# Performance work log

Measured on AMD Instinct MI355X. Metric: run time of the kernel, lower is better.

Reference implementation:

```python
import jax, jax.numpy as jnp
import numpy as np
import math

D_INPUT = 1024
D_Q = 1024
D_K = 1024
D_V = 1024
D_MODEL = 1024
B, S = 4, 2048


def setup_inputs() -> dict:
    key = jax.random.key(0)
    ks = jax.random.split(key, 9)
    sc = 0.02
    return {
        "x": jax.random.normal(ks[0], (B, S, D_INPUT), dtype=jnp.float32),
        "wq": jax.random.normal(ks[1], (D_INPUT, D_Q), dtype=jnp.float32) * sc,
        "bq": jnp.zeros((D_Q,), dtype=jnp.float32),
        "wk": jax.random.normal(ks[2], (D_INPUT, D_K), dtype=jnp.float32) * sc,
        "bk": jnp.zeros((D_K,), dtype=jnp.float32),
        "wv": jax.random.normal(ks[3], (D_INPUT, D_V), dtype=jnp.float32) * sc,
        "bv": jnp.zeros((D_V,), dtype=jnp.float32),
        "wp": jax.random.normal(ks[4], (D_V, D_MODEL), dtype=jnp.float32) * sc,
        "bp": jnp.zeros((D_MODEL,), dtype=jnp.float32),
    }


def reference(x, wq, bq, wk, bk, wv, bv, wp, bp):
    scale = math.sqrt(D_K)  # NOTE: original MULTIPLIES by sqrt(d_k)
    q = x @ wq + bq  # [B,S,Dq]
    k = x @ wk + bk  # [B,S,Dk]
    v = x @ wv + bv  # [B,S,Dv]
    scores = jnp.einsum('bsd,btd->bst', q, k) * scale
    p_attn = jax.nn.softmax(scores, axis=-1)
    # dropout: inference mode (training=False) -> identity
    context = jnp.einsum('bst,btd->bsd', p_attn, v)
    output = context @ wp + bp
    return (output, p_attn)
```

## Files before the change

kernel.cpp:

```cpp
#include <hip/hip_runtime.h>

typedef unsigned short u16;
typedef short bf16x8 __attribute__((ext_vector_type(8)));
typedef float floatx4 __attribute__((ext_vector_type(4)));

static __device__ __forceinline__ u16 f2bf(float f) {
  unsigned int u = __float_as_uint(f);
  unsigned int lsb = (u >> 16) & 1u;
  u += 0x7FFFu + lsb;
  return (u16)(u >> 16);
}
static __device__ __forceinline__ float bf2f(u16 u) {
  return __uint_as_float(((unsigned int)u) << 16);
}

static __device__ __forceinline__ void gl_lds16(const u16* g, u16* l) {
  __builtin_amdgcn_global_load_lds(
      (const __attribute__((address_space(1))) void*)g,
      (__attribute__((address_space(3))) void*)l, 16, 0, 0);
}

__global__ __launch_bounds__(256)
void prep_weights(const float* __restrict__ wq, const float* __restrict__ wk,
                  const float* __restrict__ wv, const float* __restrict__ wp,
                  const float* __restrict__ bq, const float* __restrict__ bk,
                  const float* __restrict__ bv,
                  u16* __restrict__ qkvThi, u16* __restrict__ qkvTlo,
                  u16* __restrict__ wpThi, float* __restrict__ bqkv) {
  __shared__ float t[32][33];
  const int z = blockIdx.z;
  const int tid = threadIdx.x;
  if (z == 4) {
    if (blockIdx.y == 0 && blockIdx.x < 12) {
      const int i = blockIdx.x * 256 + tid;
      bqkv[i] = (i < 1024) ? bq[i] : (i < 2048) ? bk[i - 1024] : bv[i - 2048];
    }
    return;
  }
  const float* in = (z == 0) ? wq : (z == 1) ? wk : (z == 2) ? wv : wp;
  u16* hi = (z == 3) ? wpThi : (qkvThi + (size_t)z * 1024 * 1024);
  u16* lo = (z == 0) ? qkvTlo : (z == 1) ? (qkvTlo + 1024 * 1024) : (u16*)nullptr;
  const int want_lo = (z < 2);

  const int r0 = blockIdx.y * 32, c0 = blockIdx.x * 32;
  const int lr = tid >> 3;
  const int lc = (tid & 7) * 4;
  float4 v = *(const float4*)(in + (size_t)(r0 + lr) * 1024 + c0 + lc);
  t[lr][lc + 0] = v.x; t[lr][lc + 1] = v.y; t[lr][lc + 2] = v.z; t[lr][lc + 3] = v.w;
  __syncthreads();
  u16 ph[4], pl[4];
#pragma unroll
  for (int j = 0; j < 4; j++) {
    float f = t[lc + j][lr];
    ph[j] = f2bf(f);
    pl[j] = f2bf(f - bf2f(ph[j]));
  }
  const size_t o = (size_t)(c0 + lr) * 1024 + r0 + lc;
  *(uint2*)(hi + o) = *(uint2*)ph;
  if (want_lo) *(uint2*)(lo + o) = *(uint2*)pl;
}

__global__ __launch_bounds__(256)
void split_f32(const float* __restrict__ in, u16* __restrict__ hi,
               u16* __restrict__ lo) {
  const size_t i4 = ((size_t)blockIdx.x * 256 + threadIdx.x) * 4;
  float4 v = *(const float4*)(in + i4);
  float f[4] = {v.x, v.y, v.z, v.w};
  u16 ph[4], pl[4];
#pragma unroll
  for (int j = 0; j < 4; j++) {
    ph[j] = f2bf(f[j]);
    pl[j] = f2bf(f[j] - bf2f(ph[j]));
  }
  *(uint2*)(hi + i4) = *(uint2*)ph;
  *(uint2*)(lo + i4) = *(uint2*)pl;
}

template<int KB, int ASP, int BSP, int OM, int HB>
__global__ __launch_bounds__(256)
void gemm_mfma(const u16* __restrict__ Ahi, const u16* __restrict__ Alo,
               const u16* __restrict__ Bhi, const u16* __restrict__ Blo,
               const float* __restrict__ bias,
               void* __restrict__ C0, void* __restrict__ C1,
               void* __restrict__ C2, void* __restrict__ C3,
               void* __restrict__ C4,
               int N, int K, int lda, int ldb, int ldc,
               long long aB, long long bB, long long cB, float scale,
               int nsplit) {
  constexpr int CM = KB / 8 - 1;
  constexpr int RPI = 512 / KB;
  constexpr int NI = KB / 16;
  constexpr int PL = 128 * KB;
  __shared__ __align__(16) u16 As[(1 + ASP) * PL];
  __shared__ __align__(16) u16 Bs[(1 + BSP) * PL];

  const int bz = blockIdx.z;
  const u16* A0 = Ahi + (size_t)bz * aB;
  const u16* A1 = ASP ? (Alo + (size_t)bz * aB) : (const u16*)nullptr;
  const u16* B0 = Bhi + (size_t)bz * bB;
  const u16* B1 = BSP ? (Blo + (size_t)bz * bB) : (const u16*)nullptr;

  const int m0 = blockIdx.y * 128;
  const int n0 = blockIdx.x * 128;
  const bool bsplit = (ASP && BSP) ? (n0 < nsplit) : false;
  const int tid = threadIdx.x;
  const int w = tid >> 6;
  const int L = tid & 63;
  const int rr = L & 15, quad = L >> 4;
  const int wm = (w >> 1) * 64, wn = (w & 1) * 64;

  const int lrow = (KB == 32) ? (L >> 2) : (L >> 3);
  const int c3 = (L & CM) ^ ((L >> 3) & CM);
  const int srow = w * 32 + lrow;
  u16* stA = &As[w * 32 * KB];
  u16* stB = &Bs[w * 32 * KB];
  const u16* gA0 = A0 + (size_t)(m0 + srow) * lda + c3 * 8;
  const u16* gA1 = ASP ? A1 + (size_t)(m0 + srow) * lda + c3 * 8 : (const u16*)nullptr;
  const u16* gB0 = B0 + (size_t)(n0 + srow) * ldb + c3 * 8;
  const u16* gB1 = BSP ? B1 + (size_t)(n0 + srow) * ldb + c3 * 8 : (const u16*)nullptr;

  floatx4 acc[4][4] = {};

  for (int k0 = 0; k0 < K; k0 += KB) {
#pragma unroll
    for (int q = 0; q < NI; q++) {
      gl_lds16(gA0 + k0 + (size_t)q * RPI * lda, stA + q * 512);
      gl_lds16(gB0 + k0 + (size_t)q * RPI * ldb, stB + q * 512);
    }
    if (ASP && bsplit) {
#pragma unroll
      for (int q = 0; q < NI; q++)
        gl_lds16(gA1 + k0 + (size_t)q * RPI * lda, stA + PL + q * 512);
    }
    if (BSP && bsplit) {
#pragma unroll
      for (int q = 0; q < NI; q++)
        gl_lds16(gB1 + k0 + (size_t)q * RPI * ldb, stB + PL + q * 512);
    }
    __syncthreads();

#pragma unroll
    for (int s = 0; s < KB / 32; s++) {
      const int pcb = (KB == 32) ? (quad ^ ((rr >> 1) & 3)) * 8
                                 : ((s * 4 + quad) ^ (rr & 7)) * 8;
      bf16x8 a0[4], a1[4], b0[4], b1[4];
#pragma unroll
      for (int i = 0; i < 4; i++) {
        const int arow = wm + i * 16 + rr;
        const int brow = wn + i * 16 + rr;
        a0[i] = *(const bf16x8*)&As[arow * KB + pcb];
        b0[i] = *(const bf16x8*)&Bs[brow * KB + pcb];
        if (ASP && BSP) {
          if (bsplit) {
            a1[i] = *(const bf16x8*)&As[PL + arow * KB + pcb];
            b1[i] = *(const bf16x8*)&Bs[PL + brow * KB + pcb];
          }
        }
      }
#pragma unroll
      for (int i = 0; i < 4; i++) {
#pragma unroll
        for (int j = 0; j < 4; j++) {
          acc[i][j] = __builtin_amdgcn_mfma_f32_16x16x32_bf16(a0[i], b0[j], acc[i][j], 0, 0, 0);
          if (ASP && BSP) {
            if (bsplit) {
              acc[i][j] = __builtin_amdgcn_mfma_f32_16x16x32_bf16(a0[i], b1[j], acc[i][j], 0, 0, 0);
              acc[i][j] = __builtin_amdgcn_mfma_f32_16x16x32_bf16(a1[i], b0[j], acc[i][j], 0, 0, 0);
            }
          }
        }
      }
    }
    __syncthreads();
  }

#pragma unroll
  for (int i = 0; i < 4; i++) {
    const int mbase = m0 + wm + i * 16 + quad * 4;
#pragma unroll
    for (int j = 0; j < 4; j++) {
      const int col = n0 + wn + j * 16 + rr;
      float bvs = 0.f;
      if (HB) bvs = bias[col];
      if (OM == 4) {
        if (col < 2048) {
          u16* hi; u16* lo;
          if (col < 1024) { hi = (u16*)C0; lo = (u16*)C1; }
          else            { hi = (u16*)C2; lo = (u16*)C3; }
          const int cc = col & 1023;
#pragma unroll
          for (int ii = 0; ii < 4; ii++) {
            const float v = acc[i][j][ii] + bvs;
            const size_t idx = (size_t)(mbase + ii) * 1024 + cc;
            const u16 h = f2bf(v);
            hi[idx] = h;
            lo[idx] = f2bf(v - bf2f(h));
          }
        } else {
          const int d = col - 2048;
          u16 pk[4];
#pragma unroll
          for (int ii = 0; ii < 4; ii++) pk[ii] = f2bf(acc[i][j][ii] + bvs);
          const size_t idx = (size_t)(mbase >> 11) * (2048 * 1024) +
                             (size_t)d * 2048 + (mbase & 2047);
          *(uint2*)((u16*)C4 + idx) = *(uint2*)pk;
        }
      } else {
        u16* Cb = (u16*)C0 + (size_t)bz * cB;
        float* Cf = (float*)C0 + (size_t)bz * cB;
#pragma unroll
        for (int ii = 0; ii < 4; ii++) {
          const float v = acc[i][j][ii] * scale + bvs;
          const size_t idx = (size_t)(mbase + ii) * ldc + col;
          if (OM == 0) Cb[idx] = f2bf(v);
          else         Cf[idx] = v;
        }
      }
    }
  }
}

__global__ __launch_bounds__(256)
void softmax_rows(float* __restrict__ S, u16* __restrict__ Pb) {
  const int row = blockIdx.x;
  float* s = S + (size_t)row * 2048;
  const int tid = threadIdx.x;
  const int w = tid >> 6;
  __shared__ float redm[4];
  __shared__ float reds[4];

  float v[8];
  float mx = -1e30f;
#pragma unroll
  for (int i = 0; i < 8; i++) {
    v[i] = s[tid + 256 * i];
    mx = fmaxf(mx, v[i]);
  }
#pragma unroll
  for (int o = 32; o > 0; o >>= 1) mx = fmaxf(mx, __shfl_xor(mx, o, 64));
  if ((tid & 63) == 0) redm[w] = mx;
  __syncthreads();
  mx = fmaxf(fmaxf(redm[0], redm[1]), fmaxf(redm[2], redm[3]));

  float sum = 0.f;
#pragma unroll
  for (int i = 0; i < 8; i++) {
    v[i] = __expf(v[i] - mx);
    sum += v[i];
  }
#pragma unroll
  for (int o = 32; o > 0; o >>= 1) sum += __shfl_xor(sum, o, 64);
  if ((tid & 63) == 0) reds[w] = sum;
  __syncthreads();
  sum = reds[0] + reds[1] + reds[2] + reds[3];
  const float rs = 1.0f / sum;
#pragma unroll
  for (int i = 0; i < 8; i++) {
    const float p = v[i] * rs;
    s[tid + 256 * i] = p;
    Pb[(size_t)row * 2048 + tid + 256 * i] = f2bf(p);
  }
}

extern "C" void kernel_launch(void* const* d_in, const int* in_sizes, int n_in,
                              void* d_out, int out_size, void* d_ws, size_t ws_size,
                              hipStream_t stream) {
  const float* x  = (const float*)d_in[0];
  const float* wq = (const float*)d_in[1];
  const float* bq = (const float*)d_in[2];
  const float* wk = (const float*)d_in[3];
  const float* bk = (const float*)d_in[4];
  const float* wv = (const float*)d_in[5];
  const float* bv = (const float*)d_in[6];
  const float* wp = (const float*)d_in[7];
  const float* bp = (const float*)d_in[8];

  const size_t MB = 1024 * 1024;
  char* ws = (char*)d_ws;
  u16* qkvThi = (u16*)(ws + 0 * MB);
  u16* qkvTlo = (u16*)(ws + 6 * MB);
  u16* wpThi  = (u16*)(ws + 10 * MB);
  float* bqkv = (float*)(ws + 12 * MB);
  u16* xhi    = (u16*)(ws + 13 * MB);
  u16* xlo    = (u16*)(ws + 29 * MB);
  u16* qhi    = (u16*)(ws + 45 * MB);
  u16* qlo    = (u16*)(ws + 61 * MB);
  u16* khi    = (u16*)(ws + 77 * MB);
  u16* klo    = (u16*)(ws + 93 * MB);
  u16* vT     = (u16*)(ws + 109 * MB);
  u16* pbf    = khi;
  u16* ctx    = qhi;

  float* outp = (float*)d_out;
  float* scf  = (float*)d_out + 8388608;

  const dim3 blk(256);

  prep_weights<<<dim3(32, 32, 5), blk, 0, stream>>>(
      wq, wk, wv, wp, bq, bk, bv, qkvThi, qkvTlo, wpThi, bqkv);
  split_f32<<<dim3(8192), blk, 0, stream>>>(x, xhi, xlo);

  gemm_mfma<32, 1, 1, 4, 1><<<dim3(24, 64, 1), blk, 0, stream>>>(
      xhi, xlo, qkvThi, qkvTlo, bqkv, qhi, qlo, khi, klo, vT,
      3072, 1024, 1024, 1024, 0, 0, 0, 0, 1.0f, 2048);

  gemm_mfma<32, 1, 1, 2, 0><<<dim3(16, 16, 4), blk, 0, stream>>>(
      qhi, qlo, khi, klo, nullptr, scf, nullptr, nullptr, nullptr, nullptr,
      2048, 1024, 1024, 1024, 2048,
      2048LL * 1024, 2048LL * 1024, 2048LL * 2048, 32.0f, 2048);

  softmax_rows<<<dim3(8192), blk, 0, stream>>>(scf, pbf);

  gemm_mfma<64, 0, 0, 0, 0><<<dim3(8, 16, 4), blk, 0, stream>>>(
      pbf, nullptr, vT, nullptr, nullptr, ctx, nullptr, nullptr, nullptr, nullptr,
      1024, 2048, 2048, 2048, 1024,
      2048LL * 2048, 1024LL * 2048, 2048LL * 1024, 1.0f, 0);

  gemm_mfma<64, 0, 0, 2, 1><<<dim3(8, 64, 1), blk, 0, stream>>>(
      ctx, nullptr, wpThi, nullptr, bp, outp, nullptr, nullptr, nullptr, nullptr,
      1024, 1024, 1024, 1024, 1024, 0, 0, 0, 1.0f, 0);
}
```

Before: 513.1 us.

## Switch GEMMs to 32x32x16 MFMA and split fused QKV GEMM into three launches

Result: slower. 524.5 us (+2.2%).

```diff
diff --git a/kernel.cpp b/kernel.cpp
--- a/kernel.cpp
+++ b/kernel.cpp
@@ -2,7 +2,7 @@
 
 typedef unsigned short u16;
 typedef short bf16x8 __attribute__((ext_vector_type(8)));
-typedef float floatx4 __attribute__((ext_vector_type(4)));
+typedef float floatx16 __attribute__((ext_vector_type(16)));
 
 static __device__ __forceinline__ u16 f2bf(float f) {
   unsigned int u = __float_as_uint(f);
@@ -23,20 +23,11 @@
 __global__ __launch_bounds__(256)
 void prep_weights(const float* __restrict__ wq, const float* __restrict__ wk,
                   const float* __restrict__ wv, const float* __restrict__ wp,
-                  const float* __restrict__ bq, const float* __restrict__ bk,
-                  const float* __restrict__ bv,
                   u16* __restrict__ qkvThi, u16* __restrict__ qkvTlo,
-                  u16* __restrict__ wpThi, float* __restrict__ bqkv) {
+                  u16* __restrict__ wpThi) {
   __shared__ float t[32][33];
   const int z = blockIdx.z;
   const int tid = threadIdx.x;
-  if (z == 4) {
-    if (blockIdx.y == 0 && blockIdx.x < 12) {
-      const int i = blockIdx.x * 256 + tid;
-      bqkv[i] = (i < 1024) ? bq[i] : (i < 2048) ? bk[i - 1024] : bv[i - 2048];
-    }
-    return;
-  }
   const float* in = (z == 0) ? wq : (z == 1) ? wk : (z == 2) ? wv : wp;
   u16* hi = (z == 3) ? wpThi : (qkvThi + (size_t)z * 1024 * 1024);
   u16* lo = (z == 0) ? qkvTlo : (z == 1) ? (qkvTlo + 1024 * 1024) : (u16*)nullptr;
@@ -82,11 +73,8 @@
                const u16* __restrict__ Bhi, const u16* __restrict__ Blo,
                const float* __restrict__ bias,
                void* __restrict__ C0, void* __restrict__ C1,
-               void* __restrict__ C2, void* __restrict__ C3,
-               void* __restrict__ C4,
                int N, int K, int lda, int ldb, int ldc,
-               long long aB, long long bB, long long cB, float scale,
-               int nsplit) {
+               long long aB, long long bB, long long cB, float scale) {
   constexpr int CM = KB / 8 - 1;
   constexpr int RPI = 512 / KB;
   constexpr int NI = KB / 16;
@@ -102,11 +90,10 @@
 
   const int m0 = blockIdx.y * 128;
   const int n0 = blockIdx.x * 128;
-  const bool bsplit = (ASP && BSP) ? (n0 < nsplit) : false;
   const int tid = threadIdx.x;
   const int w = tid >> 6;
   const int L = tid & 63;
-  const int rr = L & 15, quad = L >> 4;
+  const int l31 = L & 31, half = L >> 5;
   const int wm = (w >> 1) * 64, wn = (w & 1) * 64;
 
   const int lrow = (KB == 32) ? (L >> 2) : (L >> 3);
@@ -119,7 +106,7 @@
   const u16* gB0 = B0 + (size_t)(n0 + srow) * ldb + c3 * 8;
   const u16* gB1 = BSP ? B1 + (size_t)(n0 + srow) * ldb + c3 * 8 : (const u16*)nullptr;
 
-  floatx4 acc[4][4] = {};
+  floatx16 acc[2][2] = {};
 
   for (int k0 = 0; k0 < K; k0 += KB) {
 #pragma unroll
@@ -127,12 +114,12 @@
       gl_lds16(gA0 + k0 + (size_t)q * RPI * lda, stA + q * 512);
       gl_lds16(gB0 + k0 + (size_t)q * RPI * ldb, stB + q * 512);
     }
-    if (ASP && bsplit) {
+    if (ASP) {
 #pragma unroll
       for (int q = 0; q < NI; q++)
         gl_lds16(gA1 + k0 + (size_t)q * RPI * lda, stA + PL + q * 512);
     }
-    if (BSP && bsplit) {
+    if (BSP) {
 #pragma unroll
       for (int q = 0; q < NI; q++)
         gl_lds16(gB1 + k0 + (size_t)q * RPI * ldb, stB + PL + q * 512);
@@ -140,80 +127,68 @@
     __syncthreads();
 
 #pragma unroll
-    for (int s = 0; s < KB / 32; s++) {
-      const int pcb = (KB == 32) ? (quad ^ ((rr >> 1) & 3)) * 8
-                                 : ((s * 4 + quad) ^ (rr & 7)) * 8;
-      bf16x8 a0[4], a1[4], b0[4], b1[4];
-#pragma unroll
-      for (int i = 0; i < 4; i++) {
-        const int arow = wm + i * 16 + rr;
-        const int brow = wn + i * 16 + rr;
-        a0[i] = *(const bf16x8*)&As[arow * KB + pcb];
-        b0[i] = *(const bf16x8*)&Bs[brow * KB + pcb];
-        if (ASP && BSP) {
-          if (bsplit) {
-            a1[i] = *(const bf16x8*)&As[PL + arow * KB + pcb];
-            b1[i] = *(const bf16x8*)&Bs[PL + brow * KB + pcb];
+    for (int s = 0; s < KB / 16; s++) {
+      const int pcb = ((KB == 32) ? ((s * 2 + half) ^ ((l31 >> 1) & 3))
+                                  : ((s * 2 + half) ^ (l31 & 7))) * 8;
+      bf16x8 a0[2], a1[2], b0[2], b1[2];
+#pragma unroll
+      for (int i = 0; i < 2; i++) {
+        a0[i] = *(const bf16x8*)&As[(wm + i * 32 + l31) * KB + pcb];
+        b0[i] = *(const bf16x8*)&Bs[(wn + i * 32 + l31) * KB + pcb];
+        if (ASP) a1[i] = *(const bf16x8*)&As[PL + (wm + i * 32 + l31) * KB + pcb];
+        if (BSP) b1[i] = *(const bf16x8*)&Bs[PL + (wn + i * 32 + l31) * KB + pcb];
+      }
+#pragma unroll
+      for (int i = 0; i < 2; i++) {
+#pragma unroll
+        for (int j = 0; j < 2; j++) {
+          acc[i][j] = __builtin_amdgcn_mfma_f32_32x32x16_bf16(a0[i], b0[j], acc[i][j], 0, 0, 0);
+          if (ASP && BSP) {
+            acc[i][j] = __builtin_amdgcn_mfma_f32_32x32x16_bf16(a0[i], b1[j], acc[i][j], 0, 0, 0);
+            acc[i][j] = __builtin_amdgcn_mfma_f32_32x32x16_bf16(a1[i], b0[j], acc[i][j], 0, 0, 0);
           }
         }
       }
-#pragma unroll
-      for (int i = 0; i < 4; i++) {
-#pragma unroll
-        for (int j = 0; j < 4; j++) {
-          acc[i][j] = __builtin_amdgcn_mfma_f32_16x16x32_bf16(a0[i], b0[j], acc[i][j], 0, 0, 0);
-          if (ASP && BSP) {
-            if (bsplit) {
-              acc[i][j] = __builtin_amdgcn_mfma_f32_16x16x32_bf16(a0[i], b1[j], acc[i][j], 0, 0, 0);
-              acc[i][j] = __builtin_amdgcn_mfma_f32_16x16x32_bf16(a1[i], b0[j], acc[i][j], 0, 0, 0);
+    }
+    __syncthreads();
+  }
+
+#pragma unroll
+  for (int i = 0; i < 2; i++) {
+#pragma unroll
+    for (int j = 0; j < 2; j++) {
+      const int col = n0 + wn + j * 32 + l31;
+      float bvs = 0.f;
+      if (HB) bvs = bias[col];
+#pragma unroll
+      for (int rq = 0; rq < 4; rq++) {
+        const int mb = m0 + wm + i * 32 + rq * 8 + half * 4;
+        if (OM == 3) {
+          u16 pk[4];
+#pragma unroll
+          for (int ri = 0; ri < 4; ri++)
+            pk[ri] = f2bf(acc[i][j][rq * 4 + ri] * scale + bvs);
+          const size_t idx = (size_t)(mb >> 11) * (2048 * 1024) +
+                             (size_t)col * 2048 + (mb & 2047);
+          *(uint2*)((u16*)C0 + idx) = *(uint2*)pk;
+        } else {
+          u16* Cb = (u16*)C0 + (size_t)bz * cB;
+          float* Cf = (float*)C0 + (size_t)bz * cB;
+          u16* Cl = (OM == 1) ? ((u16*)C1 + (size_t)bz * cB) : (u16*)nullptr;
+#pragma unroll
+          for (int ri = 0; ri < 4; ri++) {
+            const float v = acc[i][j][rq * 4 + ri] * scale + bvs;
+            const size_t idx = (size_t)(mb + ri) * ldc + col;
+            if (OM == 0) {
+              Cb[idx] = f2bf(v);
+            } else if (OM == 1) {
+              const u16 h = f2bf(v);
+              Cb[idx] = h;
+              Cl[idx] = f2bf(v - bf2f(h));
+            } else {
+              Cf[idx] = v;
             }
           }
-        }
-      }
-    }
-    __syncthreads();
-  }
-
-#pragma unroll
-  for (int i = 0; i < 4; i++) {
-    const int mbase = m0 + wm + i * 16 + quad * 4;
-#pragma unroll
-    for (int j = 0; j < 4; j++) {
-      const int col = n0 + wn + j * 16 + rr;
-      float bvs = 0.f;
-      if (HB) bvs = bias[col];
-      if (OM == 4) {
-        if (col < 2048) {
-          u16* hi; u16* lo;
-          if (col < 1024) { hi = (u16*)C0; lo = (u16*)C1; }
-          else            { hi = (u16*)C2; lo = (u16*)C3; }
-          const int cc = col & 1023;
-#pragma unroll
-          for (int ii = 0; ii < 4; ii++) {
-            const float v = acc[i][j][ii] + bvs;
-            const size_t idx = (size_t)(mbase + ii) * 1024 + cc;
-            const u16 h = f2bf(v);
-            hi[idx] = h;
-            lo[idx] = f2bf(v - bf2f(h));
-          }
-        } else {
-          const int d = col - 2048;
-          u16 pk[4];
-#pragma unroll
-          for (int ii = 0; ii < 4; ii++) pk[ii] = f2bf(acc[i][j][ii] + bvs);
-          const size_t idx = (size_t)(mbase >> 11) * (2048 * 1024) +
-                             (size_t)d * 2048 + (mbase & 2047);
-          *(uint2*)((u16*)C4 + idx) = *(uint2*)pk;
-        }
-      } else {
-        u16* Cb = (u16*)C0 + (size_t)bz * cB;
-        float* Cf = (float*)C0 + (size_t)bz * cB;
-#pragma unroll
-        for (int ii = 0; ii < 4; ii++) {
-          const float v = acc[i][j][ii] * scale + bvs;
-          const size_t idx = (size_t)(mbase + ii) * ldc + col;
-          if (OM == 0) Cb[idx] = f2bf(v);
-          else         Cf[idx] = v;
         }
       }
     }
@@ -280,7 +255,6 @@
   u16* qkvThi = (u16*)(ws + 0 * MB);
   u16* qkvTlo = (u16*)(ws + 6 * MB);
   u16* wpThi  = (u16*)(ws + 10 * MB);
-  float* bqkv = (float*)(ws + 12 * MB);
   u16* xhi    = (u16*)(ws + 13 * MB);
   u16* xlo    = (u16*)(ws + 29 * MB);
   u16* qhi    = (u16*)(ws + 45 * MB);
@@ -296,27 +270,33 @@
 
   const dim3 blk(256);
 
-  prep_weights<<<dim3(32, 32, 5), blk, 0, stream>>>(
-      wq, wk, wv, wp, bq, bk, bv, qkvThi, qkvTlo, wpThi, bqkv);
+  prep_weights<<<dim3(32, 32, 4), blk, 0, stream>>>(
+      wq, wk, wv, wp, qkvThi, qkvTlo, wpThi);
   split_f32<<<dim3(8192), blk, 0, stream>>>(x, xhi, xlo);
 
-  gemm_mfma<32, 1, 1, 4, 1><<<dim3(24, 64, 1), blk, 0, stream>>>(
-      xhi, xlo, qkvThi, qkvTlo, bqkv, qhi, qlo, khi, klo, vT,
-      3072, 1024, 1024, 1024, 0, 0, 0, 0, 1.0f, 2048);
+  gemm_mfma<32, 1, 1, 1, 1><<<dim3(8, 64, 1), blk, 0, stream>>>(
+      xhi, xlo, qkvThi, qkvTlo, bq, qhi, qlo,
+      1024, 1024, 1024, 1024, 1024, 0, 0, 0, 1.0f);
+  gemm_mfma<32, 1, 1, 1, 1><<<dim3(8, 64, 1), blk, 0, stream>>>(
+      xhi, xlo, qkvThi + 1024 * 1024, qkvTlo + 1024 * 1024, bk, khi, klo,
+      1024, 1024, 1024, 1024, 1024, 0, 0, 0, 1.0f);
+  gemm_mfma<32, 0, 0, 3, 1><<<dim3(8, 64, 1), blk, 0, stream>>>(
+      xhi, nullptr, qkvThi + 2 * 1024 * 1024, nullptr, bv, vT, nullptr,
+      1024, 1024, 1024, 1024, 0, 0, 0, 0, 1.0f);
 
   gemm_mfma<32, 1, 1, 2, 0><<<dim3(16, 16, 4), blk, 0, stream>>>(
-      qhi, qlo, khi, klo, nullptr, scf, nullptr, nullptr, nullptr, nullptr,
+      qhi, qlo, khi, klo, nullptr, scf, nullptr,
       2048, 1024, 1024, 1024, 2048,
-      2048LL * 1024, 2048LL * 1024, 2048LL * 2048, 32.0f, 2048);
+      2048LL * 1024, 2048LL * 1024, 2048LL * 2048, 32.0f);
 
   softmax_rows<<<dim3(8192), blk, 0, stream>>>(scf, pbf);
 
   gemm_mfma<64, 0, 0, 0, 0><<<dim3(8, 16, 4), blk, 0, stream>>>(
-      pbf, nullptr, vT, nullptr, nullptr, ctx, nullptr, nullptr, nullptr, nullptr,
+      pbf, nullptr, vT, nullptr, nullptr, ctx, nullptr,
       1024, 2048, 2048, 2048, 1024,
-      2048LL * 2048, 1024LL * 2048, 2048LL * 1024, 1.0f, 0);
+      2048LL * 2048, 1024LL * 2048, 2048LL * 1024, 1.0f);
 
   gemm_mfma<64, 0, 0, 2, 1><<<dim3(8, 64, 1), blk, 0, stream>>>(
-      ctx, nullptr, wpThi, nullptr, bp, outp, nullptr, nullptr, nullptr, nullptr,
-      1024, 1024, 1024, 1024, 1024, 0, 0, 0, 1.0f, 0);
-}
+      ctx, nullptr, wpThi, nullptr, bp, outp, nullptr,
+      1024, 1024, 1024, 1024, 1024, 0, 0, 0, 1.0f);
+}
```
